# Kernel optimization log

Hardware: AMD Instinct MI355X
Metric: run time of the kernel (lower is better)

Reference implementation:

```python
import jax, jax.numpy as jnp
import numpy as np

NUM_HEADS = 32
HEAD_DIM = 128
NUM_KV_HEADS = 8
SCALE = HEAD_DIM ** -0.5
SNAPKV_LIMIT = 512   # context.snapkv_limit
SAMPLE_Q = 128       # context.snapkv_sample_queries default
B = 4                # number of sequences (uniform length)
L = 1024             # tokens per sequence
NUM_SLOTS = 8192
NEG = jnp.float32(-1e30)


def setup_inputs() -> dict:
    key = jax.random.key(0)
    k0, k1, k2 = jax.random.split(key, 3)
    N = B * L
    q = jax.random.normal(k0, (N, NUM_HEADS, HEAD_DIM), jnp.float32)
    k = jax.random.normal(k1, (N, NUM_KV_HEADS, HEAD_DIM), jnp.float32)
    v = jax.random.normal(k2, (N, NUM_KV_HEADS, HEAD_DIM), jnp.float32)
    D = NUM_KV_HEADS * HEAD_DIM
    k_cache = jnp.zeros((NUM_SLOTS, D), jnp.float32)
    v_cache = jnp.zeros((NUM_SLOTS, D), jnp.float32)
    slot_mapping = jnp.arange(N, dtype=jnp.int32)
    cu_seqlens = jnp.arange(B + 1, dtype=jnp.int32) * L
    return dict(q=q, k=k, v=v, k_cache=k_cache, v_cache=v_cache,
                slot_mapping=slot_mapping, cu_seqlens=cu_seqlens)


def _forward(q, k, v, k_cache, v_cache, slot_mapping, cu_seqlens):
    N, H, Dh = q.shape
    Hkv = k.shape[1]
    rep = H // Hkv
    nb = cu_seqlens.shape[0] - 1
    Ls = N // nb  # uniform seq length
    qb = q.reshape(nb, Ls, H, Dh)
    kb = k.reshape(nb, Ls, Hkv, Dh)
    vb = v.reshape(nb, Ls, Hkv, Dh)

    # ---- SnapKV selection (per sequence, vectorized over batch) ----
    q_s = qb[:, Ls - SAMPLE_Q:]                       # [B, SQ, H, Dh] last queries
    k_rep = jnp.repeat(kb, rep, axis=2)               # GQA expand -> [B, L, H, Dh]
    logits = jnp.einsum('bqhd,bkhd->bhqk', q_s, k_rep) * SCALE
    abs_q = jnp.arange(Ls - SAMPLE_Q, Ls)
    abs_k = jnp.arange(Ls)
    allowed = abs_k[None, :] <= abs_q[:, None]        # [SQ, L] causal for sampled q
    logits = jnp.where(allowed[None, None], logits, NEG)
    attn = jax.nn.softmax(logits, axis=-1)
    importance = attn.sum(axis=(1, 2))                # [B, L] sum over heads+queries
    _, idx = jax.lax.top_k(importance, SNAPKV_LIMIT)
    keep_idx = jnp.sort(idx, axis=-1)                 # [B, limit] sorted kept positions

    # ---- compact KV-cache store (store_kvcache on kept tokens) ----
    kept_k = jnp.take_along_axis(kb, keep_idx[:, :, None, None], axis=1)  # [B,limit,Hkv,Dh]
    kept_v = jnp.take_along_axis(vb, keep_idx[:, :, None, None], axis=1)
    # compact slots: first num_kept (= limit) slots of each sequence
    slots = slot_mapping.reshape(nb, Ls)[:, :SNAPKV_LIMIT].reshape(-1)
    D = Hkv * Dh
    k_cache_new = k_cache.at[slots].set(kept_k.reshape(-1, D))
    v_cache_new = v_cache.at[slots].set(kept_v.reshape(-1, D))

    # ---- prefill attention (flash_attn_varlen_func, causal, raw k/v) ----
    v_rep = jnp.repeat(vb, rep, axis=2)               # [B, L, H, Dh]
    scores = jnp.einsum('bqhd,bkhd->bhqk', qb, k_rep) * SCALE
    causal = abs_k[None, :] <= abs_k[:, None]         # [L, L]
    scores = jnp.where(causal[None, None], scores, NEG)
    p = jax.nn.softmax(scores, axis=-1)
    o = jnp.einsum('bhqk,bkhd->bqhd', p, v_rep).reshape(N, H, Dh)
    return o, k_cache_new, v_cache_new


def reference(q, k, v, k_cache, v_cache, slot_mapping, cu_seqlens):
    return _forward(q, k, v, k_cache, v_cache, slot_mapping, cu_seqlens)
```

## Files before the change

kernel.cpp:

```cpp
#include <hip/hip_runtime.h>

#define B_ 4
#define L_ 1024
#define H_ 32
#define HKV_ 8
#define DH_ 128
#define SCALE_ 0.08838834764831845f
#define M_FIX 20.0f
#define KEEP_ 512
#define O_ELEMS (B_*L_*H_*DH_)
#define CACHE_ELEMS (8192*HKV_*DH_)
#define TILE_US 8192
#define QTAB_US 2097152

typedef short short8 __attribute__((ext_vector_type(8)));
typedef float floatx4 __attribute__((ext_vector_type(4)));
typedef unsigned int uintx2 __attribute__((ext_vector_type(2)));
typedef unsigned int uintx4 __attribute__((ext_vector_type(4)));

__device__ inline unsigned short bf16r(float x) {
    unsigned int u = __builtin_bit_cast(unsigned int, x);
    u += 0x7fffu + ((u >> 16) & 1u);
    return (unsigned short)(u >> 16);
}
__device__ inline unsigned int pk_bf16(float a, float b) {
    return (unsigned int)bf16r(a) | ((unsigned int)bf16r(b) << 16);
}
__device__ inline float bf16tof(unsigned short h) {
    unsigned int u = ((unsigned int)h) << 16;
    return __builtin_bit_cast(float, u);
}

__global__ __launch_bounds__(256)
void convert_kernel(const float* __restrict__ Kp, const float* __restrict__ Vp,
                    unsigned short* __restrict__ Kb, unsigned short* __restrict__ Klo,
                    unsigned short* __restrict__ VTb)
{
    int bid = blockIdx.x;
    int kt = bid & 15, hkv = (bid >> 4) & 7, b = bid >> 7;
    int t = threadIdx.x;
    size_t tile = (size_t)bid * TILE_US;

    #pragma unroll
    for (int i = 0; i < 4; ++i) {
        int pos = t + 256 * i;
        int col = pos >> 4, gd = pos & 15;
        const float* kb = &Kp[((size_t)(b * L_ + kt * 64 + col) * HKV_ + hkv) * DH_ + gd * 8];
        float x[8];
        *(float4*)&x[0] = *(const float4*)kb;
        *(float4*)&x[4] = *(const float4*)(kb + 4);
        unsigned int gh[4], gl[4];
        #pragma unroll
        for (int j = 0; j < 4; ++j) {
            unsigned short h0 = bf16r(x[2*j]),   h1 = bf16r(x[2*j+1]);
            unsigned short l0 = bf16r(x[2*j]   - bf16tof(h0));
            unsigned short l1 = bf16r(x[2*j+1] - bf16tof(h1));
            gh[j] = (unsigned int)h0 | ((unsigned int)h1 << 16);
            gl[j] = (unsigned int)l0 | ((unsigned int)l1 << 16);
        }
        int phys = gd ^ (col & 15);
        *(uintx4*)&Kb[tile + col * 128 + phys * 8]  = (uintx4){gh[0], gh[1], gh[2], gh[3]};
        *(uintx4*)&Klo[tile + col * 128 + phys * 8] = (uintx4){gl[0], gl[1], gl[2], gl[3]};
    }

    {
        int d4g = t & 31, g = t >> 5;
        const float* vb = &Vp[((size_t)(b * L_ + kt * 64 + g * 8) * HKV_ + hkv) * DH_ + d4g * 4];
        const size_t vs = (size_t)HKV_ * DH_;
        float4 r[8];
        #pragma unroll
        for (int j = 0; j < 8; ++j) r[j] = *(const float4*)(vb + (size_t)j * vs);
        #pragma unroll
        for (int ii = 0; ii < 4; ++ii) {
            int d = d4g * 4 + ii;
            int phys = g ^ (d & 7);
            uintx4 gp;
            gp[0] = pk_bf16(((const float*)&r[0])[ii], ((const float*)&r[1])[ii]);
            gp[1] = pk_bf16(((const float*)&r[2])[ii], ((const float*)&r[3])[ii]);
            gp[2] = pk_bf16(((const float*)&r[4])[ii], ((const float*)&r[5])[ii]);
            gp[3] = pk_bf16(((const float*)&r[6])[ii], ((const float*)&r[7])[ii]);
            *(uintx4*)&VTb[tile + d * 64 + phys * 8] = gp;
        }
    }
}

__global__ __launch_bounds__(256)
void qconv_kernel(const float* __restrict__ Qp,
                  unsigned short* __restrict__ Qh, unsigned short* __restrict__ Ql)
{
    int bid = blockIdx.x;
    int qts = bid & 1;
    int h   = (bid >> 1) & 31;
    int b   = bid >> 6;
    int t = threadIdx.x;
    int w = t >> 6;
    int l = t & 63;
    int lm = l & 15;
    int hq = l >> 4;
    int q0 = 896 + qts * 64;

    const float* qb = Qp + ((size_t)(b * L_ + q0 + w * 16 + lm) * H_ + h) * DH_;
    #pragma unroll
    for (int c = 0; c < 4; ++c) {
        int dc = hq * 8 + 32 * c;
        float x[8];
        *(float4*)&x[0] = *(const float4*)(qb + dc);
        *(float4*)&x[4] = *(const float4*)(qb + dc + 4);
        short8 fh, fl;
        #pragma unroll
        for (int j = 0; j < 8; ++j) {
            float xs = x[j] * SCALE_;
            unsigned short hb = bf16r(xs);
            fh[j] = (short)hb;
            fl[j] = (short)bf16r(xs - bf16tof(hb));
        }
        size_t idx = (((size_t)bid * 4 + c) * 256 + t) * 8;
        *(short8*)&Qh[idx] = fh;
        *(short8*)&Ql[idx] = fl;
    }
}

__global__ __launch_bounds__(256, 4)
void attn_mfma(const float* __restrict__ Qp, const unsigned short* __restrict__ Kbp,
               const unsigned short* __restrict__ VTp, float* __restrict__ Op)
{
    __shared__ __align__(16) unsigned short k_lds[64 * 128];
    __shared__ __align__(16) unsigned short vT[128 * 64];
    __shared__ __align__(16) unsigned short p_lds[4 * 1024];

    int bid = blockIdx.x;
    int pr = bid & 7;
    int h  = (bid >> 3) & 31;
    int b  = bid >> 8;
    int hkv = h >> 2;
    int t = threadIdx.x;
    int w = t >> 6;
    int l = t & 63;
    int lm = l & 15;
    int hq = l >> 4;

    for (int ph = 0; ph < 2; ++ph) {
        int qt = ph ? (15 - pr) : pr;

        short8 aq[4];
        {
            const float* qb = Qp + ((size_t)(b * L_ + qt * 64 + w * 16 + lm) * H_ + h) * DH_;
            #pragma unroll
            for (int c = 0; c < 4; ++c) {
                int dc = hq * 8 + 32 * c;
                float4 x0 = *(const float4*)(qb + dc);
                float4 x1 = *(const float4*)(qb + dc + 4);
                uintx4 packed;
                packed[0] = pk_bf16(x0.x * SCALE_, x0.y * SCALE_);
                packed[1] = pk_bf16(x0.z * SCALE_, x0.w * SCALE_);
                packed[2] = pk_bf16(x1.x * SCALE_, x1.y * SCALE_);
                packed[3] = pk_bf16(x1.z * SCALE_, x1.w * SCALE_);
                aq[c] = __builtin_bit_cast(short8, packed);
            }
        }

        floatx4 O[8];
        #pragma unroll
        for (int n = 0; n < 8; ++n) O[n] = (floatx4){0.f, 0.f, 0.f, 0.f};
        float l_acc[4] = {0.f, 0.f, 0.f, 0.f};

        for (int kt = 0; kt <= qt; ++kt) {
            __syncthreads();
            size_t tbase = (size_t)((b * HKV_ + hkv) * 16 + kt) * TILE_US;
            {
                const uintx4* kg = (const uintx4*)(Kbp + tbase) + t;
                const uintx4* vg = (const uintx4*)(VTp + tbase) + t;
                uintx4* kd = (uintx4*)k_lds + t;
                uintx4* vd = (uintx4*)vT + t;
                #pragma unroll
                for (int i = 0; i < 4; ++i) {
                    kd[i * 256] = kg[i * 256];
                    vd[i * 256] = vg[i * 256];
                }
            }
            __syncthreads();

            floatx4 S[4];
            #pragma unroll
            for (int c = 0; c < 4; ++c) S[c] = (floatx4){-M_FIX, -M_FIX, -M_FIX, -M_FIX};
            #pragma unroll
            for (int kc = 0; kc < 4; ++kc) {
                #pragma unroll
                for (int c = 0; c < 4; ++c) {
                    int row = lm * 4 + c;
                    int phys = (kc * 4 + hq) ^ (row & 15);
                    short8 bk = *(const short8*)&k_lds[row * 128 + phys * 8];
                    S[c] = __builtin_amdgcn_mfma_f32_16x16x32_bf16(aq[kc], bk, S[c], 0, 0, 0);
                }
            }
            bool diag = (kt == qt);
            #pragma unroll
            for (int r = 0; r < 4; ++r) {
                float e0 = __expf(S[0][r]);
                float e1 = __expf(S[1][r]);
                float e2 = __expf(S[2][r]);
                float e3 = __expf(S[3][r]);
                if (diag) {
                    int qabs = qt * 64 + w * 16 + hq * 4 + r;
                    int kb0 = kt * 64 + lm * 4;
                    e0 = (kb0 + 0 <= qabs) ? e0 : 0.f;
                    e1 = (kb0 + 1 <= qabs) ? e1 : 0.f;
                    e2 = (kb0 + 2 <= qabs) ? e2 : 0.f;
                    e3 = (kb0 + 3 <= qabs) ? e3 : 0.f;
                }
                l_acc[r] += (e0 + e1) + (e2 + e3);
                int m = hq * 4 + r;
                int phys = (lm >> 1) ^ (m & 7);
                uintx2 gp;
                gp[0] = pk_bf16(e0, e1);
                gp[1] = pk_bf16(e2, e3);
                *(uintx2*)&p_lds[w * 1024 + m * 64 + phys * 8 + (lm & 1) * 4] = gp;
            }
            asm volatile("" ::: "memory");
            int phys0 = hq ^ (lm & 7);
            int phys1 = (4 + hq) ^ (lm & 7);
            short8 bp0 = *(const short8*)&p_lds[w * 1024 + lm * 64 + phys0 * 8];
            short8 bp1 = *(const short8*)&p_lds[w * 1024 + lm * 64 + phys1 * 8];
            #pragma unroll
            for (int n = 0; n < 8; ++n) {
                int d = n * 16 + lm;
                short8 a0 = *(const short8*)&vT[d * 64 + (hq ^ (d & 7)) * 8];
                O[n] = __builtin_amdgcn_mfma_f32_16x16x32_bf16(a0, bp0, O[n], 0, 0, 0);
                short8 a1 = *(const short8*)&vT[d * 64 + (((4 + hq) ^ (d & 7))) * 8];
                O[n] = __builtin_amdgcn_mfma_f32_16x16x32_bf16(a1, bp1, O[n], 0, 0, 0);
            }
        }
        #pragma unroll
        for (int r = 0; r < 4; ++r) {
            l_acc[r] += __shfl_xor(l_acc[r], 1);
            l_acc[r] += __shfl_xor(l_acc[r], 2);
            l_acc[r] += __shfl_xor(l_acc[r], 4);
            l_acc[r] += __shfl_xor(l_acc[r], 8);
        }
        float* lf = (float*)&p_lds[w * 1024];
        if (lm == 0) {
            #pragma unroll
            for (int r = 0; r < 4; ++r) lf[hq * 4 + r] = l_acc[r];
        }
        asm volatile("" ::: "memory");
        __builtin_amdgcn_wave_barrier();
        float invl = 1.0f / lf[lm];
        #pragma unroll
        for (int n = 0; n < 8; ++n) {
            float4 res;
            res.x = O[n][0] * invl; res.y = O[n][1] * invl;
            res.z = O[n][2] * invl; res.w = O[n][3] * invl;
            *(float4*)&Op[((size_t)(b * L_ + qt * 64 + w * 16 + lm) * H_ + h) * DH_ + n * 16 + hq * 4] = res;
        }
    }
}

__global__ __launch_bounds__(256, 2)
void imp_l_kernel(const unsigned short* __restrict__ Qhp, const unsigned short* __restrict__ Qlp,
                  const unsigned short* __restrict__ Kbp, const unsigned short* __restrict__ Klop,
                  float* __restrict__ invL)
{
    __shared__ __align__(16) unsigned short khi[64 * 128];
    __shared__ __align__(16) unsigned short klo[64 * 128];

    int bid = blockIdx.x;
    int qts = bid & 1;
    int h   = (bid >> 1) & 31;
    int b   = bid >> 6;
    int hkv = h >> 2;
    int t = threadIdx.x;
    int w = t >> 6;
    int l = t & 63;
    int lm = l & 15;
    int hq = l >> 4;
    int q0 = 896 + qts * 64;
    int ktd = q0 >> 6;

    short8 aqh[4], aql[4];
    #pragma unroll
    for (int c = 0; c < 4; ++c) {
        size_t idx = (((size_t)bid * 4 + c) * 256 + t) * 8;
        aqh[c] = *(const short8*)&Qhp[idx];
        aql[c] = *(const short8*)&Qlp[idx];
    }

    float l_acc[4] = {0.f, 0.f, 0.f, 0.f};
    for (int kt = 0; kt <= ktd; ++kt) {
        __syncthreads();
        size_t tbase = (size_t)((b * HKV_ + hkv) * 16 + kt) * TILE_US;
        {
            const uintx4* hg = (const uintx4*)(Kbp + tbase) + t;
            const uintx4* lg = (const uintx4*)(Klop + tbase) + t;
            uintx4* hd = (uintx4*)khi + t;
            uintx4* ld = (uintx4*)klo + t;
            #pragma unroll
            for (int i = 0; i < 4; ++i) {
                hd[i * 256] = hg[i * 256];
                ld[i * 256] = lg[i * 256];
            }
        }
        __syncthreads();

        floatx4 S[4];
        #pragma unroll
        for (int c = 0; c < 4; ++c) S[c] = (floatx4){-M_FIX, -M_FIX, -M_FIX, -M_FIX};
        #pragma unroll
        for (int kc = 0; kc < 4; ++kc) {
            #pragma unroll
            for (int c = 0; c < 4; ++c) {
                int row = lm * 4 + c;
                int phys = (kc * 4 + hq) ^ (row & 15);
                short8 bh = *(const short8*)&khi[row * 128 + phys * 8];
                short8 bl = *(const short8*)&klo[row * 128 + phys * 8];
                S[c] = __builtin_amdgcn_mfma_f32_16x16x32_bf16(aqh[kc], bh, S[c], 0, 0, 0);
                S[c] = __builtin_amdgcn_mfma_f32_16x16x32_bf16(aqh[kc], bl, S[c], 0, 0, 0);
                S[c] = __builtin_amdgcn_mfma_f32_16x16x32_bf16(aql[kc], bh, S[c], 0, 0, 0);
            }
        }
        bool diag = (kt == ktd);
        #pragma unroll
        for (int r = 0; r < 4; ++r) {
            int qabs = q0 + w * 16 + hq * 4 + r;
            #pragma unroll
            for (int c = 0; c < 4; ++c) {
                float ev = __expf(S[c][r]);
                if (diag) {
                    int kabs = kt * 64 + lm * 4 + c;
                    ev = (kabs <= qabs) ? ev : 0.f;
                }
                l_acc[r] += ev;
            }
        }
    }
    #pragma unroll
    for (int r = 0; r < 4; ++r) {
        l_acc[r] += __shfl_xor(l_acc[r], 1);
        l_acc[r] += __shfl_xor(l_acc[r], 2);
        l_acc[r] += __shfl_xor(l_acc[r], 4);
        l_acc[r] += __shfl_xor(l_acc[r], 8);
    }
    if (lm == 0) {
        #pragma unroll
        for (int r = 0; r < 4; ++r)
            invL[((size_t)(b * H_ + h)) * 128 + qts * 64 + w * 16 + hq * 4 + r] = 1.0f / l_acc[r];
    }
}

__global__ __launch_bounds__(256, 4)
void imp_col_kernel(const unsigned short* __restrict__ Qhp, const unsigned short* __restrict__ Qlp,
                    const unsigned short* __restrict__ Kbp, const unsigned short* __restrict__ Klop,
                    const float* __restrict__ invL, float* __restrict__ imp)
{
    __shared__ __align__(16) unsigned short khi[64 * 128];
    __shared__ __align__(16) unsigned short klo[64 * 128];
    __shared__ float imp_loc[64];

    int bid = blockIdx.x;
    int kt = bid & 15;
    int h  = (bid >> 4) & 31;
    int b  = bid >> 9;
    int hkv = h >> 2;
    int t = threadIdx.x;
    int w = t >> 6;
    int l = t & 63;
    int lm = l & 15;
    int hq = l >> 4;

    if (t < 64) imp_loc[t] = 0.f;
    size_t tbase = (size_t)((b * HKV_ + hkv) * 16 + kt) * TILE_US;
    {
        const uintx4* hg = (const uintx4*)(Kbp + tbase) + t;
        const uintx4* lg = (const uintx4*)(Klop + tbase) + t;
        uintx4* hd = (uintx4*)khi + t;
        uintx4* ld = (uintx4*)klo + t;
        #pragma unroll
        for (int i = 0; i < 4; ++i) {
            hd[i * 256] = hg[i * 256];
            ld[i * 256] = lg[i * 256];
        }
    }
    __syncthreads();

    float cs[4] = {0.f, 0.f, 0.f, 0.f};
    for (int qp2 = 0; qp2 < 2; ++qp2) {
        if (kt == 15 && qp2 == 0) continue;
        int q0 = 896 + qp2 * 64;
        int qbid = (b * 32 + h) * 2 + qp2;
        short8 aqh[4], aql[4];
        #pragma unroll
        for (int c = 0; c < 4; ++c) {
            size_t idx = (((size_t)qbid * 4 + c) * 256 + t) * 8;
            aqh[c] = *(const short8*)&Qhp[idx];
            aql[c] = *(const short8*)&Qlp[idx];
        }
        floatx4 iv4 = *(const floatx4*)&invL[((size_t)(b * H_ + h)) * 128 + qp2 * 64 + w * 16 + hq * 4];

        floatx4 S[4];
        #pragma unroll
        for (int c = 0; c < 4; ++c) S[c] = (floatx4){-M_FIX, -M_FIX, -M_FIX, -M_FIX};
        #pragma unroll
        for (int kc = 0; kc < 4; ++kc) {
            #pragma unroll
            for (int c = 0; c < 4; ++c) {
                int row = lm * 4 + c;
                int phys = (kc * 4 + hq) ^ (row & 15);
                short8 bh = *(const short8*)&khi[row * 128 + phys * 8];
                short8 bl = *(const short8*)&klo[row * 128 + phys * 8];
                S[c] = __builtin_amdgcn_mfma_f32_16x16x32_bf16(aqh[kc], bh, S[c], 0, 0, 0);
                S[c] = __builtin_amdgcn_mfma_f32_16x16x32_bf16(aqh[kc], bl, S[c], 0, 0, 0);
                S[c] = __builtin_amdgcn_mfma_f32_16x16x32_bf16(aql[kc], bh, S[c], 0, 0, 0);
            }
        }
        #pragma unroll
        for (int c = 0; c < 4; ++c) {
            int kabs = kt * 64 + lm * 4 + c;
            #pragma unroll
            for (int r = 0; r < 4; ++r) {
                int qabs = q0 + w * 16 + hq * 4 + r;
                float ev = (kabs <= qabs) ? __expf(S[c][r]) : 0.f;
                cs[c] += ev * iv4[r];
            }
        }
    }
    #pragma unroll
    for (int c = 0; c < 4; ++c) {
        cs[c] += __shfl_xor(cs[c], 16);
        cs[c] += __shfl_xor(cs[c], 32);
    }
    if (l < 16) {
        #pragma unroll
        for (int c = 0; c < 4; ++c) atomicAdd(&imp_loc[lm * 4 + c], cs[c]);
    }
    __syncthreads();
    if (t < 64) atomicAdd(&imp[b * L_ + kt * 64 + t], imp_loc[t]);
}

__global__ void topk_kernel(const float* __restrict__ imp, int* __restrict__ keep)
{
    __shared__ float vals[1024];
    __shared__ int   idxs[1024];
    int b = blockIdx.x;
    int t = threadIdx.x;
    for (int i = t; i < 1024; i += 512) { vals[i] = imp[b * L_ + i]; idxs[i] = i; }

    for (int size = 2; size <= 1024; size <<= 1) {
        for (int stride = size >> 1; stride > 0; stride >>= 1) {
            __syncthreads();
            for (int i = t; i < 1024; i += 512) {
                int j = i ^ stride;
                if (j > i) {
                    float vi = vals[i], vj = vals[j];
                    int ii = idxs[i], ij = idxs[j];
                    bool j_before_i = (vj > vi) || (vj == vi && ij < ii);
                    bool descRegion = ((i & size) == 0);
                    bool doSwap = descRegion ? j_before_i : !j_before_i;
                    if (doSwap) {
                        vals[i] = vj; vals[j] = vi;
                        idxs[i] = ij; idxs[j] = ii;
                    }
                }
            }
        }
    }
    __syncthreads();
    for (int size = 2; size <= 512; size <<= 1) {
        for (int stride = size >> 1; stride > 0; stride >>= 1) {
            __syncthreads();
            int i = t, j = t ^ stride;
            if (j > i) {
                int a = idxs[i], bb = idxs[j];
                bool ascRegion = ((i & size) == 0);
                bool doSwap = ascRegion ? (a > bb) : (a < bb);
                if (doSwap) { idxs[i] = bb; idxs[j] = a; }
            }
        }
    }
    __syncthreads();
    keep[b * KEEP_ + t] = idxs[t];
}

__global__ __launch_bounds__(256)
void cache_copy_kernel(const float* __restrict__ kc_in, const float* __restrict__ vc_in,
                       float* __restrict__ kc_out, float* __restrict__ vc_out)
{
    size_t idx = (size_t)blockIdx.x * 256 + threadIdx.x;
    const float4* ki = (const float4*)kc_in;
    const float4* vi = (const float4*)vc_in;
    float4* ko = (float4*)kc_out;
    float4* vo = (float4*)vc_out;
    #pragma unroll
    for (int i = 0; i < 4; ++i) {
        size_t off = idx + (size_t)i * 524288;
        ko[off] = ki[off];
        vo[off] = vi[off];
    }
}

__global__ void scatter_kernel(const float* __restrict__ kin, const float* __restrict__ vin,
                               const int* __restrict__ keep, const int* __restrict__ slot_mapping,
                               float* __restrict__ kc_out, float* __restrict__ vc_out)
{
    int bid = blockIdx.x;
    int b = bid >> 9, j = bid & 511;
    int src = b * L_ + keep[b * KEEP_ + j];
    int dst = slot_mapping[b * L_ + j];
    int t = threadIdx.x;
    float4 kv = *(const float4*)&kin[(size_t)src * 1024 + t * 4];
    *(float4*)&kc_out[(size_t)dst * 1024 + t * 4] = kv;
    float4 vv = *(const float4*)&vin[(size_t)src * 1024 + t * 4];
    *(float4*)&vc_out[(size_t)dst * 1024 + t * 4] = vv;
}

extern "C" void kernel_launch(void* const* d_in, const int* in_sizes, int n_in,
                              void* d_out, int out_size, void* d_ws, size_t ws_size,
                              hipStream_t stream)
{
    const float* q = (const float*)d_in[0];
    const float* k = (const float*)d_in[1];
    const float* v = (const float*)d_in[2];
    const float* k_cache = (const float*)d_in[3];
    const float* v_cache = (const float*)d_in[4];
    const int* slot_mapping = (const int*)d_in[5];

    float* o = (float*)d_out;
    float* kc_out = o + O_ELEMS;
    float* vc_out = kc_out + CACHE_ELEMS;

    float* imp  = (float*)d_ws;
    int*   keep = (int*)(imp + B_ * L_);
    float* invL = (float*)(keep + B_ * KEEP_);

    const size_t SCRATCH_US = (size_t)3 * 512 * TILE_US + (size_t)2 * QTAB_US;
    bool ws_fits = ws_size >= (size_t)(96 * 1024) + SCRATCH_US * sizeof(unsigned short);
    unsigned short* Kb = ws_fits ? (unsigned short*)((char*)d_ws + 96 * 1024)
                                 : (unsigned short*)vc_out;
    unsigned short* Klo = Kb  + (size_t)512 * TILE_US;
    unsigned short* VTb = Klo + (size_t)512 * TILE_US;
    unsigned short* Qh  = VTb + (size_t)512 * TILE_US;
    unsigned short* Ql  = Qh  + (size_t)QTAB_US;

    (void)hipMemsetAsync(imp, 0, B_ * L_ * 4, stream);

    convert_kernel<<<dim3(512), dim3(256), 0, stream>>>(k, v, Kb, Klo, VTb);
    qconv_kernel<<<dim3(256), dim3(256), 0, stream>>>(q, Qh, Ql);
    attn_mfma<<<dim3(1024), dim3(256), 0, stream>>>(q, Kb, VTb, o);
    imp_l_kernel<<<dim3(256), dim3(256), 0, stream>>>(Qh, Ql, Kb, Klo, invL);
    imp_col_kernel<<<dim3(2048), dim3(256), 0, stream>>>(Qh, Ql, Kb, Klo, invL, imp);
    topk_kernel<<<dim3(4), dim3(512), 0, stream>>>(imp, keep);

    cache_copy_kernel<<<dim3(2048), dim3(256), 0, stream>>>(k_cache, v_cache, kc_out, vc_out);
    scatter_kernel<<<dim3(2048), dim3(256), 0, stream>>>(k, v, keep, slot_mapping, kc_out, vc_out);
}
```

Measured before the change: 424.1 us.

## Prefetch next K/V tile into registers, fuse Q conversion, remap blocks for XCD locality

The attention and importance kernels now load the next K/V tile from global memory into registers while the current tile is being computed, so the global load overlaps the MFMA work instead of stalling before each LDS store. The separate Q-conversion kernel is folded into the K/V convert kernel, removing one launch. Block indices are permuted so that blocks sharing a KV head land on the same XCD (blockIdx & 7 interleave), which should improve L2 reuse. s_setprio is raised around the compute section. The cost is higher register pressure from the prefetch buffers, which may lower occupancy under launch_bounds(256,4).

```diff
diff --git a/kernel.cpp b/kernel.cpp
--- a/kernel.cpp
+++ b/kernel.cpp
@@ -33,8 +33,10 @@
 
 __global__ __launch_bounds__(256)
 void convert_kernel(const float* __restrict__ Kp, const float* __restrict__ Vp,
+                    const float* __restrict__ Qp,
                     unsigned short* __restrict__ Kb, unsigned short* __restrict__ Klo,
-                    unsigned short* __restrict__ VTb)
+                    unsigned short* __restrict__ VTb,
+                    unsigned short* __restrict__ Qh, unsigned short* __restrict__ Ql)
 {
     int bid = blockIdx.x;
     int kt = bid & 15, hkv = (bid >> 4) & 7, b = bid >> 7;
@@ -82,41 +84,32 @@
             *(uintx4*)&VTb[tile + d * 64 + phys * 8] = gp;
         }
     }
-}
-
-__global__ __launch_bounds__(256)
-void qconv_kernel(const float* __restrict__ Qp,
-                  unsigned short* __restrict__ Qh, unsigned short* __restrict__ Ql)
-{
-    int bid = blockIdx.x;
-    int qts = bid & 1;
-    int h   = (bid >> 1) & 31;
-    int b   = bid >> 6;
-    int t = threadIdx.x;
-    int w = t >> 6;
-    int l = t & 63;
-    int lm = l & 15;
-    int hq = l >> 4;
-    int q0 = 896 + qts * 64;
-
-    const float* qb = Qp + ((size_t)(b * L_ + q0 + w * 16 + lm) * H_ + h) * DH_;
-    #pragma unroll
-    for (int c = 0; c < 4; ++c) {
-        int dc = hq * 8 + 32 * c;
-        float x[8];
-        *(float4*)&x[0] = *(const float4*)(qb + dc);
-        *(float4*)&x[4] = *(const float4*)(qb + dc + 4);
-        short8 fh, fl;
-        #pragma unroll
-        for (int j = 0; j < 8; ++j) {
-            float xs = x[j] * SCALE_;
-            unsigned short hb = bf16r(xs);
-            fh[j] = (short)hb;
-            fl[j] = (short)bf16r(xs - bf16tof(hb));
-        }
-        size_t idx = (((size_t)bid * 4 + c) * 256 + t) * 8;
-        *(short8*)&Qh[idx] = fh;
-        *(short8*)&Ql[idx] = fl;
+
+    if (bid < 256) {
+        int qts = bid & 1;
+        int h   = (bid >> 1) & 31;
+        int qb_ = bid >> 6;
+        int w = t >> 6, l = t & 63, lm = l & 15, hq = l >> 4;
+        int q0 = 896 + qts * 64;
+        const float* qb = Qp + ((size_t)(qb_ * L_ + q0 + w * 16 + lm) * H_ + h) * DH_;
+        #pragma unroll
+        for (int c = 0; c < 4; ++c) {
+            int dc = hq * 8 + 32 * c;
+            float x[8];
+            *(float4*)&x[0] = *(const float4*)(qb + dc);
+            *(float4*)&x[4] = *(const float4*)(qb + dc + 4);
+            short8 fh, fl;
+            #pragma unroll
+            for (int j = 0; j < 8; ++j) {
+                float xs = x[j] * SCALE_;
+                unsigned short hb = bf16r(xs);
+                fh[j] = (short)hb;
+                fl[j] = (short)bf16r(xs - bf16tof(hb));
+            }
+            size_t idx = (((size_t)bid * 4 + c) * 256 + t) * 8;
+            *(short8*)&Qh[idx] = fh;
+            *(short8*)&Ql[idx] = fl;
+        }
     }
 }
 
@@ -128,7 +121,7 @@
     __shared__ __align__(16) unsigned short vT[128 * 64];
     __shared__ __align__(16) unsigned short p_lds[4 * 1024];
 
-    int bid = blockIdx.x;
+    int bid = (blockIdx.x & 7) * 128 + (blockIdx.x >> 3);
     int pr = bid & 7;
     int h  = (bid >> 3) & 31;
     int b  = bid >> 8;
@@ -159,6 +152,15 @@
             }
         }
 
+        uintx4 kpre[4], vpre[4];
+        {
+            size_t tb0 = (size_t)((b * HKV_ + hkv) * 16 + 0) * TILE_US;
+            const uintx4* kg = (const uintx4*)(Kbp + tb0) + t;
+            const uintx4* vg = (const uintx4*)(VTp + tb0) + t;
+            #pragma unroll
+            for (int i = 0; i < 4; ++i) { kpre[i] = kg[i * 256]; vpre[i] = vg[i * 256]; }
+        }
+
         floatx4 O[8];
         #pragma unroll
         for (int n = 0; n < 8; ++n) O[n] = (floatx4){0.f, 0.f, 0.f, 0.f};
@@ -166,20 +168,22 @@
 
         for (int kt = 0; kt <= qt; ++kt) {
             __syncthreads();
-            size_t tbase = (size_t)((b * HKV_ + hkv) * 16 + kt) * TILE_US;
             {
-                const uintx4* kg = (const uintx4*)(Kbp + tbase) + t;
-                const uintx4* vg = (const uintx4*)(VTp + tbase) + t;
                 uintx4* kd = (uintx4*)k_lds + t;
                 uintx4* vd = (uintx4*)vT + t;
                 #pragma unroll
-                for (int i = 0; i < 4; ++i) {
-                    kd[i * 256] = kg[i * 256];
-                    vd[i * 256] = vg[i * 256];
-                }
+                for (int i = 0; i < 4; ++i) { kd[i * 256] = kpre[i]; vd[i * 256] = vpre[i]; }
             }
             __syncthreads();
-
+            if (kt < qt) {
+                size_t tb = (size_t)((b * HKV_ + hkv) * 16 + kt + 1) * TILE_US;
+                const uintx4* kg = (const uintx4*)(Kbp + tb) + t;
+                const uintx4* vg = (const uintx4*)(VTp + tb) + t;
+                #pragma unroll
+                for (int i = 0; i < 4; ++i) { kpre[i] = kg[i * 256]; vpre[i] = vg[i * 256]; }
+            }
+
+            __builtin_amdgcn_s_setprio(1);
             floatx4 S[4];
             #pragma unroll
             for (int c = 0; c < 4; ++c) S[c] = (floatx4){-M_FIX, -M_FIX, -M_FIX, -M_FIX};
@@ -229,6 +233,7 @@
                 short8 a1 = *(const short8*)&vT[d * 64 + (((4 + hq) ^ (d & 7))) * 8];
                 O[n] = __builtin_amdgcn_mfma_f32_16x16x32_bf16(a1, bp1, O[n], 0, 0, 0);
             }
+            __builtin_amdgcn_s_setprio(0);
         }
         #pragma unroll
         for (int r = 0; r < 4; ++r) {
@@ -263,7 +268,7 @@
     __shared__ __align__(16) unsigned short khi[64 * 128];
     __shared__ __align__(16) unsigned short klo[64 * 128];
 
-    int bid = blockIdx.x;
+    int bid = (blockIdx.x & 7) * 32 + (blockIdx.x >> 3);
     int qts = bid & 1;
     int h   = (bid >> 1) & 31;
     int b   = bid >> 6;
@@ -284,22 +289,32 @@
         aql[c] = *(const short8*)&Qlp[idx];
     }
 
+    size_t tabbase = (size_t)((b * HKV_ + hkv) * 16) * TILE_US;
+    uintx4 hpre[4], lpre[4];
+    {
+        const uintx4* hg = (const uintx4*)(Kbp + tabbase) + t;
+        const uintx4* lg = (const uintx4*)(Klop + tabbase) + t;
+        #pragma unroll
+        for (int i = 0; i < 4; ++i) { hpre[i] = hg[i * 256]; lpre[i] = lg[i * 256]; }
+    }
+
     float l_acc[4] = {0.f, 0.f, 0.f, 0.f};
     for (int kt = 0; kt <= ktd; ++kt) {
         __syncthreads();
-        size_t tbase = (size_t)((b * HKV_ + hkv) * 16 + kt) * TILE_US;
         {
-            const uintx4* hg = (const uintx4*)(Kbp + tbase) + t;
-            const uintx4* lg = (const uintx4*)(Klop + tbase) + t;
             uintx4* hd = (uintx4*)khi + t;
             uintx4* ld = (uintx4*)klo + t;
             #pragma unroll
-            for (int i = 0; i < 4; ++i) {
-                hd[i * 256] = hg[i * 256];
-                ld[i * 256] = lg[i * 256];
-            }
+            for (int i = 0; i < 4; ++i) { hd[i * 256] = hpre[i]; ld[i * 256] = lpre[i]; }
         }
         __syncthreads();
+        if (kt < ktd) {
+            size_t tb = tabbase + (size_t)(kt + 1) * TILE_US;
+            const uintx4* hg = (const uintx4*)(Kbp + tb) + t;
+            const uintx4* lg = (const uintx4*)(Klop + tb) + t;
+            #pragma unroll
+            for (int i = 0; i < 4; ++i) { hpre[i] = hg[i * 256]; lpre[i] = lg[i * 256]; }
+        }
 
         floatx4 S[4];
         #pragma unroll
@@ -355,7 +370,7 @@
     __shared__ __align__(16) unsigned short klo[64 * 128];
     __shared__ float imp_loc[64];
 
-    int bid = blockIdx.x;
+    int bid = (blockIdx.x & 7) * 256 + (blockIdx.x >> 3);
     int kt = bid & 15;
     int h  = (bid >> 4) & 31;
     int b  = bid >> 9;
@@ -541,8 +556,7 @@
 
     (void)hipMemsetAsync(imp, 0, B_ * L_ * 4, stream);
 
-    convert_kernel<<<dim3(512), dim3(256), 0, stream>>>(k, v, Kb, Klo, VTb);
-    qconv_kernel<<<dim3(256), dim3(256), 0, stream>>>(q, Qh, Ql);
+    convert_kernel<<<dim3(512), dim3(256), 0, stream>>>(k, v, q, Kb, Klo, VTb, Qh, Ql);
     attn_mfma<<<dim3(1024), dim3(256), 0, stream>>>(q, Kb, VTb, o);
     imp_l_kernel<<<dim3(256), dim3(256), 0, stream>>>(Qh, Ql, Kb, Klo, invL);
     imp_col_kernel<<<dim3(2048), dim3(256), 0, stream>>>(Qh, Ql, Kb, Klo, invL, imp);
```

After: 456.2 us. 7.5% more time.

## Fuse Q conversion into K/V convert kernel and merge cache copy with scatter

Applied to the files above, without the earlier changes.

Folds the Q bf16 hi/lo split into the first 256 blocks of the K/V convert kernel, which removes one launch. Topk now also writes an inverse slot map (slot to source token). A single cache_out kernel then writes each output cache row once, from either the new k/v or the old cache, instead of copying the whole cache and then scattering over it. This saves a launch and the redundant writes of scattered rows, at the cost of an extra memset and a workspace layout shift.

```diff
diff --git a/kernel.cpp b/kernel.cpp
--- a/kernel.cpp
+++ b/kernel.cpp
@@ -33,8 +33,10 @@
 
 __global__ __launch_bounds__(256)
 void convert_kernel(const float* __restrict__ Kp, const float* __restrict__ Vp,
+                    const float* __restrict__ Qp,
                     unsigned short* __restrict__ Kb, unsigned short* __restrict__ Klo,
-                    unsigned short* __restrict__ VTb)
+                    unsigned short* __restrict__ VTb,
+                    unsigned short* __restrict__ Qh, unsigned short* __restrict__ Ql)
 {
     int bid = blockIdx.x;
     int kt = bid & 15, hkv = (bid >> 4) & 7, b = bid >> 7;
@@ -82,41 +84,32 @@
             *(uintx4*)&VTb[tile + d * 64 + phys * 8] = gp;
         }
     }
-}
-
-__global__ __launch_bounds__(256)
-void qconv_kernel(const float* __restrict__ Qp,
-                  unsigned short* __restrict__ Qh, unsigned short* __restrict__ Ql)
-{
-    int bid = blockIdx.x;
-    int qts = bid & 1;
-    int h   = (bid >> 1) & 31;
-    int b   = bid >> 6;
-    int t = threadIdx.x;
-    int w = t >> 6;
-    int l = t & 63;
-    int lm = l & 15;
-    int hq = l >> 4;
-    int q0 = 896 + qts * 64;
-
-    const float* qb = Qp + ((size_t)(b * L_ + q0 + w * 16 + lm) * H_ + h) * DH_;
-    #pragma unroll
-    for (int c = 0; c < 4; ++c) {
-        int dc = hq * 8 + 32 * c;
-        float x[8];
-        *(float4*)&x[0] = *(const float4*)(qb + dc);
-        *(float4*)&x[4] = *(const float4*)(qb + dc + 4);
-        short8 fh, fl;
-        #pragma unroll
-        for (int j = 0; j < 8; ++j) {
-            float xs = x[j] * SCALE_;
-            unsigned short hb = bf16r(xs);
-            fh[j] = (short)hb;
-            fl[j] = (short)bf16r(xs - bf16tof(hb));
-        }
-        size_t idx = (((size_t)bid * 4 + c) * 256 + t) * 8;
-        *(short8*)&Qh[idx] = fh;
-        *(short8*)&Ql[idx] = fl;
+
+    if (bid < 256) {
+        int qts = bid & 1;
+        int h   = (bid >> 1) & 31;
+        int qb_ = bid >> 6;
+        int w = t >> 6, l = t & 63, lm = l & 15, hq = l >> 4;
+        int q0 = 896 + qts * 64;
+        const float* qb = Qp + ((size_t)(qb_ * L_ + q0 + w * 16 + lm) * H_ + h) * DH_;
+        #pragma unroll
+        for (int c = 0; c < 4; ++c) {
+            int dc = hq * 8 + 32 * c;
+            float x[8];
+            *(float4*)&x[0] = *(const float4*)(qb + dc);
+            *(float4*)&x[4] = *(const float4*)(qb + dc + 4);
+            short8 fh, fl;
+            #pragma unroll
+            for (int j = 0; j < 8; ++j) {
+                float xs = x[j] * SCALE_;
+                unsigned short hb = bf16r(xs);
+                fh[j] = (short)hb;
+                fl[j] = (short)bf16r(xs - bf16tof(hb));
+            }
+            size_t idx = (((size_t)bid * 4 + c) * 256 + t) * 8;
+            *(short8*)&Qh[idx] = fh;
+            *(short8*)&Ql[idx] = fl;
+        }
     }
 }
 
@@ -435,7 +428,8 @@
     if (t < 64) atomicAdd(&imp[b * L_ + kt * 64 + t], imp_loc[t]);
 }
 
-__global__ void topk_kernel(const float* __restrict__ imp, int* __restrict__ keep)
+__global__ void topk_kernel(const float* __restrict__ imp, const int* __restrict__ slot_mapping,
+                            int* __restrict__ keep, int* __restrict__ inv)
 {
     __shared__ float vals[1024];
     __shared__ int   idxs[1024];
@@ -477,6 +471,31 @@
     }
     __syncthreads();
     keep[b * KEEP_ + t] = idxs[t];
+    if (inv) {
+        int dest = slot_mapping[b * L_ + t];
+        inv[dest] = b * L_ + idxs[t];
+    }
+}
+
+__global__ __launch_bounds__(256)
+void cache_out_kernel(const float* __restrict__ kin, const float* __restrict__ vin,
+                      const float* __restrict__ kc_in, const float* __restrict__ vc_in,
+                      const int* __restrict__ inv,
+                      float* __restrict__ kc_out, float* __restrict__ vc_out)
+{
+    int bid = blockIdx.x;
+    int t = threadIdx.x;
+    #pragma unroll
+    for (int i = 0; i < 4; ++i) {
+        int s = bid * 4 + i;
+        int src = inv[s];
+        const float4* kp = (src >= 0) ? (const float4*)&kin[(size_t)src * 1024]
+                                      : (const float4*)&kc_in[(size_t)s * 1024];
+        const float4* vp = (src >= 0) ? (const float4*)&vin[(size_t)src * 1024]
+                                      : (const float4*)&vc_in[(size_t)s * 1024];
+        ((float4*)&kc_out[(size_t)s * 1024])[t] = kp[t];
+        ((float4*)&vc_out[(size_t)s * 1024])[t] = vp[t];
+    }
 }
 
 __global__ __launch_bounds__(256)
@@ -529,10 +548,13 @@
     float* imp  = (float*)d_ws;
     int*   keep = (int*)(imp + B_ * L_);
     float* invL = (float*)(keep + B_ * KEEP_);
+    int*   inv  = (int*)(invL + B_ * H_ * 128);
+    bool use_inv = ws_size >= (size_t)(120 * 1024);
+    if (!use_inv) inv = nullptr;
 
     const size_t SCRATCH_US = (size_t)3 * 512 * TILE_US + (size_t)2 * QTAB_US;
-    bool ws_fits = ws_size >= (size_t)(96 * 1024) + SCRATCH_US * sizeof(unsigned short);
-    unsigned short* Kb = ws_fits ? (unsigned short*)((char*)d_ws + 96 * 1024)
+    bool ws_fits = ws_size >= (size_t)(128 * 1024) + SCRATCH_US * sizeof(unsigned short);
+    unsigned short* Kb = ws_fits ? (unsigned short*)((char*)d_ws + 128 * 1024)
                                  : (unsigned short*)vc_out;
     unsigned short* Klo = Kb  + (size_t)512 * TILE_US;
     unsigned short* VTb = Klo + (size_t)512 * TILE_US;
@@ -540,14 +562,18 @@
     unsigned short* Ql  = Qh  + (size_t)QTAB_US;
 
     (void)hipMemsetAsync(imp, 0, B_ * L_ * 4, stream);
-
-    convert_kernel<<<dim3(512), dim3(256), 0, stream>>>(k, v, Kb, Klo, VTb);
-    qconv_kernel<<<dim3(256), dim3(256), 0, stream>>>(q, Qh, Ql);
+    if (use_inv) (void)hipMemsetAsync(inv, 0xFF, 8192 * 4, stream);
+
+    convert_kernel<<<dim3(512), dim3(256), 0, stream>>>(k, v, q, Kb, Klo, VTb, Qh, Ql);
     attn_mfma<<<dim3(1024), dim3(256), 0, stream>>>(q, Kb, VTb, o);
     imp_l_kernel<<<dim3(256), dim3(256), 0, stream>>>(Qh, Ql, Kb, Klo, invL);
     imp_col_kernel<<<dim3(2048), dim3(256), 0, stream>>>(Qh, Ql, Kb, Klo, invL, imp);
-    topk_kernel<<<dim3(4), dim3(512), 0, stream>>>(imp, keep);
-
-    cache_copy_kernel<<<dim3(2048), dim3(256), 0, stream>>>(k_cache, v_cache, kc_out, vc_out);
-    scatter_kernel<<<dim3(2048), dim3(256), 0, stream>>>(k, v, keep, slot_mapping, kc_out, vc_out);
-}
+    topk_kernel<<<dim3(4), dim3(512), 0, stream>>>(imp, slot_mapping, keep, inv);
+
+    if (use_inv) {
+        cache_out_kernel<<<dim3(2048), dim3(256), 0, stream>>>(k, v, k_cache, v_cache, inv, kc_out, vc_out);
+    } else {
+        cache_copy_kernel<<<dim3(2048), dim3(256), 0, stream>>>(k_cache, v_cache, kc_out, vc_out);
+        scatter_kernel<<<dim3(2048), dim3(256), 0, stream>>>(k, v, keep, slot_mapping, kc_out, vc_out);
+    }
+}
```

Measured after the change: 413.2 us. -2.6%, faster.
